# Kernel optimization log

Hardware: AMD Instinct MI355X
Metric: run time of the kernel (lower is better)

Reference implementation:

```python
import jax, jax.numpy as jnp
import numpy as np

SHORT_RANGE_CUTOFF = 1.6
N_PAIRS = 20_000_000
N_ATOMS = 100_000


def setup_inputs() -> dict:
    key = jax.random.key(0)
    k1, k2, k3 = jax.random.split(key, 3)
    Rij = jax.random.normal(k1, (N_PAIRS, 3), dtype=jnp.float32)
    idx_i = jax.random.randint(k2, (N_PAIRS,), 0, N_ATOMS, dtype=jnp.int64)
    idx_j = jax.random.randint(k3, (N_PAIRS,), 0, N_ATOMS, dtype=jnp.int64)
    return {"Rij": Rij, "idx_i": idx_i, "idx_j": idx_j}


def reference(Rij, idx_i, idx_j):
    """Faithful jax version of FilterShortRange.forward.

    torch.nonzero produces a dynamic-size index set; under jit we express the
    same compaction as a fixed-size stable partition: all pairs with
    ||Rij|| <= cutoff are packed to the front (original relative order
    preserved, matching torch.nonzero's ascending-index order), the tail is
    padded (Rij rows zeroed, idx entries set to -1), and n_valid reports the
    true compacted length.
    """
    rij = jnp.linalg.norm(Rij, axis=-1)                 # [P]
    mask = rij <= SHORT_RANGE_CUTOFF                    # [P] bool
    # stable argsort of ~mask: valid (False=0) entries first, order preserved
    order = jnp.argsort(jnp.logical_not(mask), stable=True)  # [P]
    mask_sorted = mask[order]                           # [P]
    Rij_sr = jnp.where(mask_sorted[:, None], Rij[order], 0.0)
    idx_i_sr = jnp.where(mask_sorted, idx_i[order], -1)
    idx_j_sr = jnp.where(mask_sorted, idx_j[order], -1)
    n_valid = jnp.sum(mask.astype(jnp.int32))
    # long-range copies are the untouched originals
    return (Rij_sr, idx_i_sr, idx_j_sr, Rij, idx_i, idx_j, n_valid)
```

## Files before the change

### kernel.cpp

```cpp
#include <hip/hip_runtime.h>
#include <math.h>


#define BLOCK 256
#define VPT 4
#define CHUNK (BLOCK * VPT)
#define SCAN_T 1024

typedef float vf4 __attribute__((ext_vector_type(4)));
typedef int vi4 __attribute__((ext_vector_type(4)));

__device__ __forceinline__ bool short_mask(float x, float y, float z) {
    float s = x * x + y * y + z * z;
    return sqrtf(s) <= 1.6f;
}

__global__ __launch_bounds__(BLOCK) void count_kernel(
    const float* __restrict__ Rij, int* __restrict__ counts, int P) {
    int b = blockIdx.x;
    int tid = threadIdx.x;
    int e0 = b * CHUNK + tid * VPT;
    int cnt = 0;
    if (e0 + VPT <= P) {
        const vf4* R4 = (const vf4*)Rij + (e0 * 3) / 4;
        vf4 a = R4[0], c = R4[1], d = R4[2];
        cnt += short_mask(a.x, a.y, a.z);
        cnt += short_mask(a.w, c.x, c.y);
        cnt += short_mask(c.z, c.w, d.x);
        cnt += short_mask(d.y, d.z, d.w);
    } else {
        for (int j = 0; j < VPT; ++j) {
            int p = e0 + j;
            if (p < P) {
                float x = Rij[3 * p], y = Rij[3 * p + 1], z = Rij[3 * p + 2];
                cnt += short_mask(x, y, z);
            }
        }
    }
    for (int off = 32; off > 0; off >>= 1) cnt += __shfl_down(cnt, off);
    __shared__ int sm[BLOCK / 64];
    int lane = tid & 63, wid = tid >> 6;
    if (lane == 0) sm[wid] = cnt;
    __syncthreads();
    if (tid == 0) {
        int t = 0;
        for (int w = 0; w < BLOCK / 64; ++w) t += sm[w];
        counts[b] = t;
    }
}

__global__ __launch_bounds__(SCAN_T) void scan_kernel(
    const int* __restrict__ counts, int* __restrict__ offsets, int nb,
    int* __restrict__ nvalid_ws, float* __restrict__ nvalid_out) {
    int tid = threadIdx.x;
    int seg = (nb + SCAN_T - 1) / SCAN_T;
    int s0 = tid * seg;
    int local = 0;
    for (int k = 0; k < seg; ++k) {
        int i = s0 + k;
        if (i < nb) local += counts[i];
    }
    int lane = tid & 63, wid = tid >> 6;
    int incl = local;
    for (int off = 1; off < 64; off <<= 1) {
        int y = __shfl_up(incl, off);
        if (lane >= off) incl += y;
    }
    __shared__ int wsum[SCAN_T / 64];
    if (lane == 63) wsum[wid] = incl;
    __syncthreads();
    int wpre = 0;
    for (int w = 0; w < wid; ++w) wpre += wsum[w];
    int run = wpre + incl - local;
    for (int k = 0; k < seg; ++k) {
        int i = s0 + k;
        if (i < nb) {
            offsets[i] = run;
            run += counts[i];
        }
    }
    if (tid == 0) {
        int tot = 0;
        for (int w = 0; w < SCAN_T / 64; ++w) tot += wsum[w];
        nvalid_ws[0] = tot;
        nvalid_out[0] = (float)tot;
    }
}

__global__ __launch_bounds__(BLOCK) void scatter_kernel(
    const float* __restrict__ Rij, const int* __restrict__ idx_i,
    const int* __restrict__ idx_j, const int* __restrict__ offsets,
    const int* __restrict__ nvalid_ws, float* __restrict__ out, int P) {
    __shared__ float rs[3 * CHUNK];
    __shared__ int iis[CHUNK];
    __shared__ int jjs[CHUNK];
    __shared__ int wsums[BLOCK / 64];

    int b = blockIdx.x;
    int tid = threadIdx.x;
    int lane = tid & 63, wid = tid >> 6;
    int e0 = b * CHUNK + tid * VPT;

    float x[VPT], y[VPT], z[VPT];
    int ii[VPT], jj[VPT];
    bool m[VPT];

    if (e0 + VPT <= P) {
        const vf4* R4 = (const vf4*)Rij + (e0 * 3) / 4;
        vf4 a = R4[0], c = R4[1], d = R4[2];
        x[0] = a.x; y[0] = a.y; z[0] = a.z;
        x[1] = a.w; y[1] = c.x; z[1] = c.y;
        x[2] = c.z; y[2] = c.w; z[2] = d.x;
        x[3] = d.y; y[3] = d.z; z[3] = d.w;
        vi4 vi = *((const vi4*)idx_i + e0 / 4);
        vi4 vj = *((const vi4*)idx_j + e0 / 4);
        ii[0] = vi.x; ii[1] = vi.y; ii[2] = vi.z; ii[3] = vi.w;
        jj[0] = vj.x; jj[1] = vj.y; jj[2] = vj.z; jj[3] = vj.w;
        for (int j = 0; j < VPT; ++j) m[j] = short_mask(x[j], y[j], z[j]);
        vf4* lrR = (vf4*)(out + 5LL * P) + (e0 * 3) / 4;
        __builtin_nontemporal_store(a, lrR + 0);
        __builtin_nontemporal_store(c, lrR + 1);
        __builtin_nontemporal_store(d, lrR + 2);
        vf4 fi = {(float)ii[0], (float)ii[1], (float)ii[2], (float)ii[3]};
        vf4 fj = {(float)jj[0], (float)jj[1], (float)jj[2], (float)jj[3]};
        __builtin_nontemporal_store(fi, (vf4*)(out + 8LL * P) + e0 / 4);
        __builtin_nontemporal_store(fj, (vf4*)(out + 9LL * P) + e0 / 4);
    } else {
        for (int j = 0; j < VPT; ++j) {
            int p = e0 + j;
            if (p < P) {
                x[j] = Rij[3 * p]; y[j] = Rij[3 * p + 1]; z[j] = Rij[3 * p + 2];
                ii[j] = idx_i[p]; jj[j] = idx_j[p];
                m[j] = short_mask(x[j], y[j], z[j]);
                out[5LL * P + 3 * p] = x[j];
                out[5LL * P + 3 * p + 1] = y[j];
                out[5LL * P + 3 * p + 2] = z[j];
                out[8LL * P + p] = (float)ii[j];
                out[9LL * P + p] = (float)jj[j];
            } else {
                m[j] = false;
            }
        }
    }

    int cnt = (int)m[0] + (int)m[1] + (int)m[2] + (int)m[3];

    int xs = cnt;
    for (int off = 1; off < 64; off <<= 1) {
        int yv = __shfl_up(xs, off);
        if (lane >= off) xs += yv;
    }
    int waveExcl = xs - cnt;
    if (lane == 63) wsums[wid] = xs;
    __syncthreads();
    int wpre = 0;
    for (int w = 0; w < wid; ++w) wpre += wsums[w];
    int cntB = 0;
    for (int w = 0; w < BLOCK / 64; ++w) cntB += wsums[w];

    int lv = wpre + waveExcl;
    for (int j = 0; j < VPT; ++j) {
        if (m[j]) {
            rs[3 * lv] = x[j];
            rs[3 * lv + 1] = y[j];
            rs[3 * lv + 2] = z[j];
            iis[lv] = ii[j];
            jjs[lv] = jj[j];
            ++lv;
        }
    }
    __syncthreads();

    int gbase = offsets[b];
    int nvalid = nvalid_ws[0];
    int blockStart = b * CHUNK;
    int blockN = min(CHUNK, P - blockStart);
    int invB = blockN - cntB;
    long long tailStart = (long long)nvalid + (blockStart - gbase);

    for (int k = tid; k < 3 * cntB; k += BLOCK)
        __builtin_nontemporal_store(rs[k], out + 3LL * gbase + k);
    for (int k = tid; k < cntB; k += BLOCK) {
        __builtin_nontemporal_store((float)iis[k], out + 3LL * P + gbase + k);
        __builtin_nontemporal_store((float)jjs[k], out + 4LL * P + gbase + k);
    }
    for (int k = tid; k < 3 * invB; k += BLOCK)
        __builtin_nontemporal_store(0.0f, out + 3LL * tailStart + k);
    for (int k = tid; k < invB; k += BLOCK) {
        __builtin_nontemporal_store(-1.0f, out + 3LL * P + tailStart + k);
        __builtin_nontemporal_store(-1.0f, out + 4LL * P + tailStart + k);
    }
}

extern "C" void kernel_launch(void* const* d_in, const int* in_sizes, int n_in,
                              void* d_out, int out_size, void* d_ws, size_t ws_size,
                              hipStream_t stream) {
    const float* Rij = (const float*)d_in[0];
    const int* idx_i = (const int*)d_in[1];
    const int* idx_j = (const int*)d_in[2];
    int P = in_sizes[1];
    float* out = (float*)d_out;

    int nb = (P + CHUNK - 1) / CHUNK;
    int* counts = (int*)d_ws;
    int* offsets = counts + nb;
    int* nvalid_ws = offsets + nb;

    count_kernel<<<nb, BLOCK, 0, stream>>>(Rij, counts, P);
    scan_kernel<<<1, SCAN_T, 0, stream>>>(counts, offsets, nb, nvalid_ws,
                                          out + 10LL * P);
    scatter_kernel<<<nb, BLOCK, 0, stream>>>(Rij, idx_i, idx_j, offsets,
                                             nvalid_ws, out, P);
}
```

Measured before the change: 1.205 ms.

## Replace count/scan/scatter with single-pass decoupled-lookback compaction kernel

Replaces the three-pass scheme (count kernel, single-block scan, scatter) with one fused kernel. It takes dynamic block IDs from an atomic ticket and computes block offsets through a decoupled lookback over packed flag/count words. This avoids reading Rij twice and drops the serial scan launch. The padding tail is now written by a separate grid-stride kernel. Valid elements are written directly from registers instead of being staged in shared memory, so stores are less coalesced, and lookback spinning can add latency.

```diff
diff --git a/kernel.cpp b/kernel.cpp
--- a/kernel.cpp
+++ b/kernel.cpp
@@ -5,101 +5,40 @@
 #define BLOCK 256
 #define VPT 4
 #define CHUNK (BLOCK * VPT)
-#define SCAN_T 1024
+#define TAIL_GRID 2048
 
 typedef float vf4 __attribute__((ext_vector_type(4)));
 typedef int vi4 __attribute__((ext_vector_type(4)));
+typedef unsigned long long u64;
 
 __device__ __forceinline__ bool short_mask(float x, float y, float z) {
     float s = x * x + y * y + z * z;
     return sqrtf(s) <= 1.6f;
 }
 
-__global__ __launch_bounds__(BLOCK) void count_kernel(
-    const float* __restrict__ Rij, int* __restrict__ counts, int P) {
-    int b = blockIdx.x;
-    int tid = threadIdx.x;
-    int e0 = b * CHUNK + tid * VPT;
-    int cnt = 0;
-    if (e0 + VPT <= P) {
-        const vf4* R4 = (const vf4*)Rij + (e0 * 3) / 4;
-        vf4 a = R4[0], c = R4[1], d = R4[2];
-        cnt += short_mask(a.x, a.y, a.z);
-        cnt += short_mask(a.w, c.x, c.y);
-        cnt += short_mask(c.z, c.w, d.x);
-        cnt += short_mask(d.y, d.z, d.w);
-    } else {
-        for (int j = 0; j < VPT; ++j) {
-            int p = e0 + j;
-            if (p < P) {
-                float x = Rij[3 * p], y = Rij[3 * p + 1], z = Rij[3 * p + 2];
-                cnt += short_mask(x, y, z);
-            }
-        }
-    }
-    for (int off = 32; off > 0; off >>= 1) cnt += __shfl_down(cnt, off);
-    __shared__ int sm[BLOCK / 64];
-    int lane = tid & 63, wid = tid >> 6;
-    if (lane == 0) sm[wid] = cnt;
-    __syncthreads();
-    if (tid == 0) {
-        int t = 0;
-        for (int w = 0; w < BLOCK / 64; ++w) t += sm[w];
-        counts[b] = t;
-    }
-}
-
-__global__ __launch_bounds__(SCAN_T) void scan_kernel(
-    const int* __restrict__ counts, int* __restrict__ offsets, int nb,
-    int* __restrict__ nvalid_ws, float* __restrict__ nvalid_out) {
-    int tid = threadIdx.x;
-    int seg = (nb + SCAN_T - 1) / SCAN_T;
-    int s0 = tid * seg;
-    int local = 0;
-    for (int k = 0; k < seg; ++k) {
-        int i = s0 + k;
-        if (i < nb) local += counts[i];
-    }
-    int lane = tid & 63, wid = tid >> 6;
-    int incl = local;
-    for (int off = 1; off < 64; off <<= 1) {
-        int y = __shfl_up(incl, off);
-        if (lane >= off) incl += y;
-    }
-    __shared__ int wsum[SCAN_T / 64];
-    if (lane == 63) wsum[wid] = incl;
-    __syncthreads();
-    int wpre = 0;
-    for (int w = 0; w < wid; ++w) wpre += wsum[w];
-    int run = wpre + incl - local;
-    for (int k = 0; k < seg; ++k) {
-        int i = s0 + k;
-        if (i < nb) {
-            offsets[i] = run;
-            run += counts[i];
-        }
-    }
-    if (tid == 0) {
-        int tot = 0;
-        for (int w = 0; w < SCAN_T / 64; ++w) tot += wsum[w];
-        nvalid_ws[0] = tot;
-        nvalid_out[0] = (float)tot;
-    }
-}
-
-__global__ __launch_bounds__(BLOCK) void scatter_kernel(
+__global__ void init_kernel(u64* __restrict__ state,
+                            unsigned int* __restrict__ ticket, int nb) {
+    int i = blockIdx.x * blockDim.x + threadIdx.x;
+    if (i < nb) state[i] = 0ull;
+    if (i == 0) ticket[0] = 0u;
+}
+
+__global__ __launch_bounds__(BLOCK) void fused_kernel(
     const float* __restrict__ Rij, const int* __restrict__ idx_i,
-    const int* __restrict__ idx_j, const int* __restrict__ offsets,
-    const int* __restrict__ nvalid_ws, float* __restrict__ out, int P) {
-    __shared__ float rs[3 * CHUNK];
-    __shared__ int iis[CHUNK];
-    __shared__ int jjs[CHUNK];
+    const int* __restrict__ idx_j, u64* __restrict__ state,
+    unsigned int* __restrict__ ticket, int* __restrict__ nvalid_ws,
+    float* __restrict__ out, int P, int nb) {
+    __shared__ unsigned int s_bid;
     __shared__ int wsums[BLOCK / 64];
-
-    int b = blockIdx.x;
+    __shared__ int s_excl;
+
     int tid = threadIdx.x;
     int lane = tid & 63, wid = tid >> 6;
-    int e0 = b * CHUNK + tid * VPT;
+
+    if (tid == 0) s_bid = atomicAdd(ticket, 1u);
+    __syncthreads();
+    int bid = (int)s_bid;
+    int e0 = bid * CHUNK + tid * VPT;
 
     float x[VPT], y[VPT], z[VPT];
     int ii[VPT], jj[VPT];
@@ -155,40 +94,94 @@
     __syncthreads();
     int wpre = 0;
     for (int w = 0; w < wid; ++w) wpre += wsums[w];
-    int cntB = 0;
-    for (int w = 0; w < BLOCK / 64; ++w) cntB += wsums[w];
-
-    int lv = wpre + waveExcl;
+    int cntB = wsums[0] + wsums[1] + wsums[2] + wsums[3];
+
+    if (tid == 0) {
+        u64 pk = ((u64)cntB << 2) | (bid == 0 ? 2ull : 1ull);
+        __hip_atomic_store(&state[bid], pk, __ATOMIC_RELEASE,
+                           __HIP_MEMORY_SCOPE_AGENT);
+        if (bid == 0) {
+            s_excl = 0;
+            if (nb == 1) { nvalid_ws[0] = cntB; out[10LL * P] = (float)cntB; }
+        }
+    }
+
+    if (wid == 0 && bid > 0) {
+        int running = 0;
+        int j = bid - 1;
+        for (;;) {
+            int idx = j - lane;
+            int flag; int val;
+            if (idx >= 0) {
+                u64 v;
+                do {
+                    v = __hip_atomic_load(&state[idx], __ATOMIC_ACQUIRE,
+                                          __HIP_MEMORY_SCOPE_AGENT);
+                    if ((v & 3ull) == 0ull) __builtin_amdgcn_s_sleep(1);
+                } while ((v & 3ull) == 0ull);
+                flag = (int)(v & 3ull);
+                val = (int)(v >> 2);
+            } else {
+                flag = 2; val = 0;
+            }
+            u64 bal = __ballot(flag == 2);
+            if (bal) {
+                int L = __ffsll((long long)bal) - 1;
+                int contrib = (lane <= L) ? val : 0;
+                for (int off = 32; off > 0; off >>= 1)
+                    contrib += __shfl_down(contrib, off);
+                running += __shfl(contrib, 0);
+                break;
+            } else {
+                int contrib = val;
+                for (int off = 32; off > 0; off >>= 1)
+                    contrib += __shfl_down(contrib, off);
+                running += __shfl(contrib, 0);
+                j -= 64;
+            }
+        }
+        if (lane == 0) {
+            int incl = running + cntB;
+            __hip_atomic_store(&state[bid], (((u64)incl) << 2) | 2ull,
+                               __ATOMIC_RELEASE, __HIP_MEMORY_SCOPE_AGENT);
+            s_excl = running;
+            if (bid == nb - 1) {
+                nvalid_ws[0] = incl;
+                out[10LL * P] = (float)incl;
+            }
+        }
+    }
+    __syncthreads();
+
+    int vbase = s_excl + wpre + waveExcl;
+    int thrPre = 0;
     for (int j = 0; j < VPT; ++j) {
         if (m[j]) {
-            rs[3 * lv] = x[j];
-            rs[3 * lv + 1] = y[j];
-            rs[3 * lv + 2] = z[j];
-            iis[lv] = ii[j];
-            jjs[lv] = jj[j];
-            ++lv;
-        }
-    }
-    __syncthreads();
-
-    int gbase = offsets[b];
-    int nvalid = nvalid_ws[0];
-    int blockStart = b * CHUNK;
-    int blockN = min(CHUNK, P - blockStart);
-    int invB = blockN - cntB;
-    long long tailStart = (long long)nvalid + (blockStart - gbase);
-
-    for (int k = tid; k < 3 * cntB; k += BLOCK)
-        __builtin_nontemporal_store(rs[k], out + 3LL * gbase + k);
-    for (int k = tid; k < cntB; k += BLOCK) {
-        __builtin_nontemporal_store((float)iis[k], out + 3LL * P + gbase + k);
-        __builtin_nontemporal_store((float)jjs[k], out + 4LL * P + gbase + k);
-    }
-    for (int k = tid; k < 3 * invB; k += BLOCK)
-        __builtin_nontemporal_store(0.0f, out + 3LL * tailStart + k);
-    for (int k = tid; k < invB; k += BLOCK) {
-        __builtin_nontemporal_store(-1.0f, out + 3LL * P + tailStart + k);
-        __builtin_nontemporal_store(-1.0f, out + 4LL * P + tailStart + k);
+            long long v = vbase + thrPre;
+            out[3 * v] = x[j];
+            out[3 * v + 1] = y[j];
+            out[3 * v + 2] = z[j];
+            out[3LL * P + v] = (float)ii[j];
+            out[4LL * P + v] = (float)jj[j];
+            ++thrPre;
+        }
+    }
+}
+
+__global__ __launch_bounds__(BLOCK) void tail_kernel(
+    const int* __restrict__ nvalid_ws, float* __restrict__ out, int P) {
+    long long nv = nvalid_ws[0];
+    long long tail = (long long)P - nv;
+    long long stride = (long long)gridDim.x * blockDim.x;
+    long long t0 = (long long)blockIdx.x * blockDim.x + threadIdx.x;
+    float* r0 = out + 3 * nv;
+    for (long long k = t0; k < 3 * tail; k += stride)
+        __builtin_nontemporal_store(0.0f, r0 + k);
+    float* i0 = out + 3LL * P + nv;
+    float* j0 = out + 4LL * P + nv;
+    for (long long k = t0; k < tail; k += stride) {
+        __builtin_nontemporal_store(-1.0f, i0 + k);
+        __builtin_nontemporal_store(-1.0f, j0 + k);
     }
 }
 
@@ -202,13 +195,12 @@
     float* out = (float*)d_out;
 
     int nb = (P + CHUNK - 1) / CHUNK;
-    int* counts = (int*)d_ws;
-    int* offsets = counts + nb;
-    int* nvalid_ws = offsets + nb;
-
-    count_kernel<<<nb, BLOCK, 0, stream>>>(Rij, counts, P);
-    scan_kernel<<<1, SCAN_T, 0, stream>>>(counts, offsets, nb, nvalid_ws,
-                                          out + 10LL * P);
-    scatter_kernel<<<nb, BLOCK, 0, stream>>>(Rij, idx_i, idx_j, offsets,
-                                             nvalid_ws, out, P);
-}
+    unsigned int* ticket = (unsigned int*)d_ws;
+    int* nvalid_ws = (int*)d_ws + 1;
+    u64* state = (u64*)((char*)d_ws + 8);
+
+    init_kernel<<<(nb + 255) / 256, 256, 0, stream>>>(state, ticket, nb);
+    fused_kernel<<<nb, BLOCK, 0, stream>>>(Rij, idx_i, idx_j, state, ticket,
+                                           nvalid_ws, out, P, nb);
+    tail_kernel<<<TAIL_GRID, BLOCK, 0, stream>>>(nvalid_ws, out, P);
+}
```

Result: slower. 4.095 ms (+239.8%).
